# Performance work log

Hardware: AMD Instinct MI355X
Metric: run time of the kernel (lower is better)

The kernel has to match this reference:

```python
import jax, jax.numpy as jnp
import numpy as np

N_NODES = 50000
N_EDGES = 800000
IN = 128
HID = 128
OUT = 128
EDGE_F = 2
EPS = 1e-30


def _linear_params(key, fan_in, fan_out, bias=True):
    k1, k2 = jax.random.split(key)
    bound = 1.0 / np.sqrt(fan_in)
    W = jax.random.uniform(k1, (fan_in, fan_out), jnp.float32, -bound, bound)
    if bias:
        b = jax.random.uniform(k2, (fan_out,), jnp.float32, -bound, bound)
        return W, b
    return (W,)


def setup_inputs() -> dict:
    key = jax.random.key(0)
    ks = jax.random.split(key, 12)
    node_feat = jax.random.normal(ks[0], (N_NODES, IN), jnp.float32)
    coord_feat = jax.random.normal(ks[1], (N_NODES, 3), jnp.float32)
    edge_feat = jax.random.normal(ks[2], (N_EDGES, EDGE_F), jnp.float32)
    src = jax.random.randint(ks[3], (N_EDGES,), 0, N_NODES, jnp.int32)
    dst = jax.random.randint(ks[4], (N_EDGES,), 0, N_NODES, jnp.int32)
    # edge_mlp: Linear(2*IN+EDGE_F+1 -> HID), SiLU, Linear(HID -> HID), SiLU
    eW1, eb1 = _linear_params(ks[5], 2 * IN + EDGE_F + 1, HID)
    eW2, eb2 = _linear_params(ks[6], HID, HID)
    # node_mlp: Linear(IN+HID -> HID), SiLU, Linear(HID -> OUT)
    nW1, nb1 = _linear_params(ks[7], IN + HID, HID)
    nW2, nb2 = _linear_params(ks[8], HID, OUT)
    # coord_mlp: Linear(HID -> HID), SiLU, Linear(HID -> 1, bias=False)
    cW1, cb1 = _linear_params(ks[9], HID, HID)
    (cW2,) = _linear_params(ks[10], HID, 1, bias=False)
    return {
        "node_feat": node_feat, "coord_feat": coord_feat, "edge_feat": edge_feat,
        "src": src, "dst": dst,
        "eW1": eW1, "eb1": eb1, "eW2": eW2, "eb2": eb2,
        "nW1": nW1, "nb1": nb1, "nW2": nW2, "nb2": nb2,
        "cW1": cW1, "cb1": cb1, "cW2": cW2,
    }


def reference(node_feat, coord_feat, edge_feat, src, dst,
              eW1, eb1, eW2, eb2, nW1, nb1, nW2, nb2, cW1, cb1, cW2):
    silu = jax.nn.silu
    n = node_feat.shape[0]
    # per-edge gathers (src -> dst message flow, as in DGL)
    h_src = node_feat[src]                      # [E, IN]
    h_dst = node_feat[dst]                      # [E, IN]
    x_diff = coord_feat[src] - coord_feat[dst]  # [E, 3]
    radial = jnp.sum(x_diff * x_diff, axis=1, keepdims=True)  # [E, 1]
    x_diff = x_diff / (jnp.sqrt(radial) + EPS)
    # edge MLP
    f = jnp.concatenate([h_src, h_dst, radial, edge_feat], axis=-1)  # [E, 2*IN+1+EF]
    msg_h = silu(silu(f @ eW1 + eb1) @ eW2 + eb2)                    # [E, HID]
    msg_x = (silu(msg_h @ cW1 + cb1) @ cW2) * x_diff                 # [E, 3]
    # scatter to destination nodes: sum for h, mean for x
    h_neigh = jax.ops.segment_sum(msg_h, dst, num_segments=n)        # [N, HID]
    x_sum = jax.ops.segment_sum(msg_x, dst, num_segments=n)          # [N, 3]
    deg = jax.ops.segment_sum(jnp.ones((msg_x.shape[0],), msg_x.dtype), dst, num_segments=n)
    x_neigh = x_sum / jnp.maximum(deg, 1.0)[:, None]
    # node update
    h = silu(jnp.concatenate([node_feat, h_neigh], axis=-1) @ nW1 + nb1) @ nW2 + nb2
    x = coord_feat + x_neigh
    return h, x
```

## Files before the change

kernel.cpp:

```cpp
#include <hip/hip_runtime.h>
#include <hip/hip_bf16.h>

#define N_NODES 50000
#define E_TOTAL 800000
#define IN      128
#define HID     128
#define EPB     64
#define XOFF    ((size_t)N_NODES * HID)
#define FP      296
#define H1OFF   160
#define HP      136
#define CP      264

typedef __attribute__((ext_vector_type(8))) short short8v;
typedef __attribute__((ext_vector_type(4))) float f32x4;

__device__ __forceinline__ float silu_f(float x) { return x / (1.0f + __expf(-x)); }

__device__ __forceinline__ uint pkbf(float lo, float hi) {
    float2 f; f.x = lo; f.y = hi;
    __hip_bfloat162 h = __float22bfloat162_rn(f);
    union { __hip_bfloat162 h; uint u; } c; c.h = h;
    return c.u;
}

__device__ __forceinline__ ushort f2bf(float x) {
    uint u = __float_as_uint(x);
    u += 0x7fff + ((u >> 16) & 1);
    return (ushort)(u >> 16);
}

__global__ __launch_bounds__(256) void prep_kernel(
    const float* __restrict__ eW1, const float* __restrict__ eW2,
    const float* __restrict__ cW1, const float* __restrict__ nW1,
    const float* __restrict__ nW2, const float* __restrict__ node_feat,
    ushort* __restrict__ pk1, ushort* __restrict__ pk2, ushort* __restrict__ pk3,
    ushort* __restrict__ pkn1, ushort* __restrict__ pkn2,
    ushort* __restrict__ nfb, int do_nfb)
{
    int id = blockIdx.x * 256 + threadIdx.x;
    if (id < 14848) {
        const float* W; ushort* dp; int K, idx;
        if (id < 4608)       { idx = id;         W = eW1; dp = pk1;  K = 259; }
        else if (id < 6656)  { idx = id - 4608;  W = eW2; dp = pk2;  K = 128; }
        else if (id < 8704)  { idx = id - 6656;  W = cW1; dp = pk3;  K = 128; }
        else if (id < 12800) { idx = id - 8704;  W = nW1; dp = pkn1; K = 256; }
        else                 { idx = id - 12800; W = nW2; dp = pkn2; K = 128; }
        int kt = idx >> 9, n = (idx >> 6) & 7, ll = idx & 63;
        int col = (n << 4) + (ll & 15);
        short8v o;
#pragma unroll
        for (int j = 0; j < 8; ++j) {
            int k = (kt << 5) + ((ll >> 4) << 3) + j;
            o[j] = (k < K) ? (short)f2bf(W[(size_t)k * 128 + col]) : (short)0;
        }
        *reinterpret_cast<short8v*>(dp + (size_t)idx * 8) = o;
    } else if (do_nfb) {
        int idx = id - 14848;
        if (idx < N_NODES * 16) {
            const float4* s = reinterpret_cast<const float4*>(node_feat + (size_t)idx * 8);
            float4 a = s[0], b = s[1];
            uint4 u;
            u.x = pkbf(a.x, a.y); u.y = pkbf(a.z, a.w);
            u.z = pkbf(b.x, b.y); u.w = pkbf(b.z, b.w);
            *reinterpret_cast<uint4*>(nfb + (size_t)idx * 8) = u;
        }
    }
}

template<bool NFB>
__global__ __launch_bounds__(512, 8) void edge_kernel(
    const float* __restrict__ node_feat, const ushort* __restrict__ nfb,
    const float* __restrict__ coord, const float* __restrict__ edge_feat,
    const int* __restrict__ src, const int* __restrict__ dst,
    const ushort* __restrict__ pk1, const ushort* __restrict__ pk2,
    const ushort* __restrict__ pk3,
    const float* __restrict__ eb1, const float* __restrict__ eb2,
    const float* __restrict__ cb1, const float* __restrict__ cW2,
    float* __restrict__ hacc, float* __restrict__ xacc, float* __restrict__ deg)
{
    __shared__ __attribute__((aligned(16))) ushort fbuf[EPB][FP];
    __shared__ int   sbuf[EPB], dbuf[EPB];
    __shared__ float xdbuf[EPB][4];
    __shared__ float pbuf[4][EPB];

    const int t   = threadIdx.x;
    const int l   = t & 63;
    const int w   = t >> 6;
    const int ch  = w & 3;
    const int eh  = w >> 2;
    const int r16 = l & 15;
    const int g   = l >> 4;
    const int e_base = blockIdx.x * EPB;

    if (t < EPB) { sbuf[t] = src[e_base + t]; dbuf[t] = dst[e_base + t]; }
    __syncthreads();

    {
        const int e = t >> 3;
        const int c = (t & 7) << 5;
        if (NFB) {
            const ushort* sp = (c < 128) ? nfb + (size_t)sbuf[e] * 128 + c
                                         : nfb + (size_t)dbuf[e] * 128 + (c - 128);
            const short8v* spv = reinterpret_cast<const short8v*>(sp);
#pragma unroll
            for (int i = 0; i < 4; ++i)
                *reinterpret_cast<short8v*>(&fbuf[e][c + (i << 3)]) = spv[i];
        } else {
            const float* sp = (c < 128) ? node_feat + (size_t)sbuf[e] * 128 + c
                                        : node_feat + (size_t)dbuf[e] * 128 + (c - 128);
            const float4* spv = reinterpret_cast<const float4*>(sp);
#pragma unroll
            for (int i = 0; i < 4; ++i) {
                float4 a = spv[2 * i], b = spv[2 * i + 1];
                uint4 u;
                u.x = pkbf(a.x, a.y); u.y = pkbf(a.z, a.w);
                u.z = pkbf(b.x, b.y); u.w = pkbf(b.z, b.w);
                *reinterpret_cast<uint4*>(&fbuf[e][c + (i << 3)]) = u;
            }
        }
    }
    if (t < EPB) {
        const int e = t, s = sbuf[e], d = dbuf[e];
        float dx = coord[(size_t)s*3+0] - coord[(size_t)d*3+0];
        float dy = coord[(size_t)s*3+1] - coord[(size_t)d*3+1];
        float dz = coord[(size_t)s*3+2] - coord[(size_t)d*3+2];
        float radial = dx*dx + dy*dy + dz*dz;
        float inv = 1.0f / (sqrtf(radial) + 1e-30f);
        fbuf[e][256] = f2bf(radial);
        fbuf[e][257] = f2bf(edge_feat[(size_t)(e_base + e)*2 + 0]);
        fbuf[e][258] = f2bf(edge_feat[(size_t)(e_base + e)*2 + 1]);
#pragma unroll
        for (int k = 259; k < 288; ++k) fbuf[e][k] = 0;
        xdbuf[e][0] = dx * inv; xdbuf[e][1] = dy * inv; xdbuf[e][2] = dz * inv;
    }
    __syncthreads();

    const f32x4 zero = {0.f, 0.f, 0.f, 0.f};
    const short8v* pkv1 = reinterpret_cast<const short8v*>(pk1);
    const short8v* pkv2 = reinterpret_cast<const short8v*>(pk2);
    const short8v* pkv3 = reinterpret_cast<const short8v*>(pk3);

    f32x4 acc[2][2];
    acc[0][0] = zero; acc[0][1] = zero; acc[1][0] = zero; acc[1][1] = zero;
    for (int kt = 0; kt < 9; ++kt) {
        short8v b0 = *reinterpret_cast<const short8v*>(&fbuf[(eh << 5) + r16][(kt << 5) + (g << 3)]);
        short8v b1 = *reinterpret_cast<const short8v*>(&fbuf[(eh << 5) + 16 + r16][(kt << 5) + (g << 3)]);
#pragma unroll
        for (int nt = 0; nt < 2; ++nt) {
            short8v a = pkv1[(((kt << 3) + (ch << 1) + nt) << 6) + l];
            acc[0][nt] = __builtin_amdgcn_mfma_f32_16x16x32_bf16(a, b0, acc[0][nt], 0, 0, 0);
            acc[1][nt] = __builtin_amdgcn_mfma_f32_16x16x32_bf16(a, b1, acc[1][nt], 0, 0, 0);
        }
    }
    __syncthreads();
#pragma unroll
    for (int nt = 0; nt < 2; ++nt) {
        int cb = (ch << 5) + (nt << 4) + (g << 2);
        float4 bias = *reinterpret_cast<const float4*>(&eb1[cb]);
#pragma unroll
        for (int et = 0; et < 2; ++et) {
            int e = (eh << 5) + (et << 4) + r16;
            f32x4 v = acc[et][nt];
            uint2 p;
            p.x = pkbf(silu_f(v[0] + bias.x), silu_f(v[1] + bias.y));
            p.y = pkbf(silu_f(v[2] + bias.z), silu_f(v[3] + bias.w));
            *reinterpret_cast<uint2*>(&fbuf[e][H1OFF + cb]) = p;
        }
    }
    __syncthreads();

    acc[0][0] = zero; acc[0][1] = zero; acc[1][0] = zero; acc[1][1] = zero;
    for (int kt = 0; kt < 4; ++kt) {
        short8v b0 = *reinterpret_cast<const short8v*>(&fbuf[(eh << 5) + r16][H1OFF + (kt << 5) + (g << 3)]);
        short8v b1 = *reinterpret_cast<const short8v*>(&fbuf[(eh << 5) + 16 + r16][H1OFF + (kt << 5) + (g << 3)]);
#pragma unroll
        for (int nt = 0; nt < 2; ++nt) {
            short8v a = pkv2[(((kt << 3) + (ch << 1) + nt) << 6) + l];
            acc[0][nt] = __builtin_amdgcn_mfma_f32_16x16x32_bf16(a, b0, acc[0][nt], 0, 0, 0);
            acc[1][nt] = __builtin_amdgcn_mfma_f32_16x16x32_bf16(a, b1, acc[1][nt], 0, 0, 0);
        }
    }
#pragma unroll
    for (int nt = 0; nt < 2; ++nt) {
        int cb = (ch << 5) + (nt << 4) + (g << 2);
        float4 bias = *reinterpret_cast<const float4*>(&eb2[cb]);
#pragma unroll
        for (int et = 0; et < 2; ++et) {
            int e = (eh << 5) + (et << 4) + r16;
            f32x4 v = acc[et][nt];
            uint2 p;
            p.x = pkbf(silu_f(v[0] + bias.x), silu_f(v[1] + bias.y));
            p.y = pkbf(silu_f(v[2] + bias.z), silu_f(v[3] + bias.w));
            *reinterpret_cast<uint2*>(&fbuf[e][cb]) = p;
        }
    }
    __syncthreads();

    {
        const int se = t >> 4;
        const int sc = t & 15;
#pragma unroll
        for (int p = 0; p < 2; ++p) {
            int e = se + (p << 5);
            int gd = dbuf[e];
            float* dp = hacc + (size_t)gd * HID + sc;
#pragma unroll
            for (int i = 0; i < 8; ++i) {
                ushort us = fbuf[e][sc + (i << 4)];
                atomicAdd(dp + (i << 4), __uint_as_float((uint)us << 16));
            }
        }
    }

    acc[0][0] = zero; acc[0][1] = zero; acc[1][0] = zero; acc[1][1] = zero;
    for (int kt = 0; kt < 4; ++kt) {
        short8v b0 = *reinterpret_cast<const short8v*>(&fbuf[(eh << 5) + r16][(kt << 5) + (g << 3)]);
        short8v b1 = *reinterpret_cast<const short8v*>(&fbuf[(eh << 5) + 16 + r16][(kt << 5) + (g << 3)]);
#pragma unroll
        for (int nt = 0; nt < 2; ++nt) {
            short8v a = pkv3[(((kt << 3) + (ch << 1) + nt) << 6) + l];
            acc[0][nt] = __builtin_amdgcn_mfma_f32_16x16x32_bf16(a, b0, acc[0][nt], 0, 0, 0);
            acc[1][nt] = __builtin_amdgcn_mfma_f32_16x16x32_bf16(a, b1, acc[1][nt], 0, 0, 0);
        }
    }
    float part[2] = {0.f, 0.f};
#pragma unroll
    for (int nt = 0; nt < 2; ++nt) {
        int cb = (ch << 5) + (nt << 4) + (g << 2);
        float4 bias = *reinterpret_cast<const float4*>(&cb1[cb]);
        float4 cw   = *reinterpret_cast<const float4*>(&cW2[cb]);
#pragma unroll
        for (int et = 0; et < 2; ++et) {
            f32x4 v = acc[et][nt];
            part[et] += silu_f(v[0] + bias.x) * cw.x + silu_f(v[1] + bias.y) * cw.y
                      + silu_f(v[2] + bias.z) * cw.z + silu_f(v[3] + bias.w) * cw.w;
        }
    }
#pragma unroll
    for (int et = 0; et < 2; ++et) {
        part[et] += __shfl_xor(part[et], 16);
        part[et] += __shfl_xor(part[et], 32);
    }
    if (l < 16) {
        pbuf[ch][(eh << 5) + r16]      = part[0];
        pbuf[ch][(eh << 5) + 16 + r16] = part[1];
    }
    __syncthreads();

    if (t < EPB) {
        float s = pbuf[0][t] + pbuf[1][t] + pbuf[2][t] + pbuf[3][t];
        int gd = dbuf[t];
        atomicAdd(&xacc[(size_t)gd*3 + 0], s * xdbuf[t][0]);
        atomicAdd(&xacc[(size_t)gd*3 + 1], s * xdbuf[t][1]);
        atomicAdd(&xacc[(size_t)gd*3 + 2], s * xdbuf[t][2]);
        atomicAdd(&deg[gd], 1.0f);
    }
}

template<bool NFB>
__global__ __launch_bounds__(256) void node_kernel(
    const float* __restrict__ node_feat, const ushort* __restrict__ nfb,
    const float* __restrict__ coord,
    const ushort* __restrict__ pkn1, const ushort* __restrict__ pkn2,
    const float* __restrict__ nb1, const float* __restrict__ nb2,
    float* __restrict__ dout, const float* __restrict__ deg)
{
    __shared__ __attribute__((aligned(16))) ushort catb[32][CP];
    __shared__ __attribute__((aligned(16))) ushort h1b[32][HP];

    const int t   = threadIdx.x;
    const int l   = t & 63;
    const int w   = t >> 6;
    const int ch  = w & 1;
    const int eh  = w >> 1;
    const int r16 = l & 15;
    const int g   = l >> 4;
    const int nb  = blockIdx.x * 32;

    {
        int nd = t >> 3;
        int c  = (t & 7) << 5;
        int gn = nb + nd; if (gn >= N_NODES) gn = N_NODES - 1;
        if (c < 128) {
            if (NFB) {
                const short8v* spv = reinterpret_cast<const short8v*>(nfb + (size_t)gn * 128 + c);
#pragma unroll
                for (int i = 0; i < 4; ++i)
                    *reinterpret_cast<short8v*>(&catb[nd][c + (i << 3)]) = spv[i];
            } else {
                const float4* spv = reinterpret_cast<const float4*>(node_feat + (size_t)gn * 128 + c);
#pragma unroll
                for (int i = 0; i < 4; ++i) {
                    float4 a = spv[2 * i], b = spv[2 * i + 1];
                    uint4 u;
                    u.x = pkbf(a.x, a.y); u.y = pkbf(a.z, a.w);
                    u.z = pkbf(b.x, b.y); u.w = pkbf(b.z, b.w);
                    *reinterpret_cast<uint4*>(&catb[nd][c + (i << 3)]) = u;
                }
            }
        } else {
            const float4* spv = reinterpret_cast<const float4*>(dout + (size_t)gn * HID + (c - 128));
#pragma unroll
            for (int i = 0; i < 4; ++i) {
                float4 a = spv[2 * i], b = spv[2 * i + 1];
                uint4 u;
                u.x = pkbf(a.x, a.y); u.y = pkbf(a.z, a.w);
                u.z = pkbf(b.x, b.y); u.w = pkbf(b.z, b.w);
                *reinterpret_cast<uint4*>(&catb[nd][c + (i << 3)]) = u;
            }
        }
    }
    __syncthreads();

    const f32x4 zero = {0.f, 0.f, 0.f, 0.f};
    const short8v* pv1 = reinterpret_cast<const short8v*>(pkn1);
    const short8v* pv2 = reinterpret_cast<const short8v*>(pkn2);

    f32x4 acc[4];
#pragma unroll
    for (int nt = 0; nt < 4; ++nt) acc[nt] = zero;
    for (int kt = 0; kt < 8; ++kt) {
        short8v b = *reinterpret_cast<const short8v*>(&catb[(eh << 4) + r16][(kt << 5) + (g << 3)]);
#pragma unroll
        for (int nt = 0; nt < 4; ++nt) {
            short8v a = pv1[(((kt << 3) + (ch << 2) + nt) << 6) + l];
            acc[nt] = __builtin_amdgcn_mfma_f32_16x16x32_bf16(a, b, acc[nt], 0, 0, 0);
        }
    }
#pragma unroll
    for (int nt = 0; nt < 4; ++nt) {
        int cb = (ch << 6) + (nt << 4) + (g << 2);
        float4 bias = *reinterpret_cast<const float4*>(&nb1[cb]);
        int nd = (eh << 4) + r16;
        f32x4 v = acc[nt];
        uint2 p;
        p.x = pkbf(silu_f(v[0] + bias.x), silu_f(v[1] + bias.y));
        p.y = pkbf(silu_f(v[2] + bias.z), silu_f(v[3] + bias.w));
        *reinterpret_cast<uint2*>(&h1b[nd][cb]) = p;
    }
    __syncthreads();

#pragma unroll
    for (int nt = 0; nt < 4; ++nt) acc[nt] = zero;
    for (int kt = 0; kt < 4; ++kt) {
        short8v b = *reinterpret_cast<const short8v*>(&h1b[(eh << 4) + r16][(kt << 5) + (g << 3)]);
#pragma unroll
        for (int nt = 0; nt < 4; ++nt) {
            short8v a = pv2[(((kt << 3) + (ch << 2) + nt) << 6) + l];
            acc[nt] = __builtin_amdgcn_mfma_f32_16x16x32_bf16(a, b, acc[nt], 0, 0, 0);
        }
    }
    {
        int gw = nb + (eh << 4) + r16;
        if (gw < N_NODES) {
#pragma unroll
            for (int nt = 0; nt < 4; ++nt) {
                int cb = (ch << 6) + (nt << 4) + (g << 2);
                float4 bias = *reinterpret_cast<const float4*>(&nb2[cb]);
                f32x4 v = acc[nt];
                float4 o;
                o.x = v[0] + bias.x; o.y = v[1] + bias.y;
                o.z = v[2] + bias.z; o.w = v[3] + bias.w;
                *reinterpret_cast<float4*>(&dout[(size_t)gw * HID + cb]) = o;
            }
        }
    }

    if (t < 96) {
        int nd = t / 3, d = t - 3 * nd;
        int gn = nb + nd;
        if (gn < N_NODES) {
            size_t xi = XOFF + (size_t)gn * 3 + d;
            float dg = deg[gn];
            dg = dg > 1.0f ? dg : 1.0f;
            dout[xi] = coord[(size_t)gn * 3 + d] + dout[xi] / dg;
        }
    }
}

extern "C" void kernel_launch(void* const* d_in, const int* in_sizes, int n_in,
                              void* d_out, int out_size, void* d_ws, size_t ws_size,
                              hipStream_t stream) {
    const float* node_feat = (const float*)d_in[0];
    const float* coord     = (const float*)d_in[1];
    const float* edge_feat = (const float*)d_in[2];
    const int*   src       = (const int*)d_in[3];
    const int*   dst       = (const int*)d_in[4];
    const float* eW1 = (const float*)d_in[5];
    const float* eb1 = (const float*)d_in[6];
    const float* eW2 = (const float*)d_in[7];
    const float* eb2 = (const float*)d_in[8];
    const float* nW1 = (const float*)d_in[9];
    const float* nb1 = (const float*)d_in[10];
    const float* nW2 = (const float*)d_in[11];
    const float* nb2 = (const float*)d_in[12];
    const float* cW1 = (const float*)d_in[13];
    const float* cb1 = (const float*)d_in[14];
    const float* cW2 = (const float*)d_in[15];

    float* out = (float*)d_out;
    float* deg = (float*)d_ws;
    char* base = (char*)d_ws;
    ushort* pk1  = (ushort*)(base + 200000);
    ushort* pk2  = (ushort*)(base + 273728);
    ushort* pk3  = (ushort*)(base + 306496);
    ushort* pkn1 = (ushort*)(base + 339264);
    ushort* pkn2 = (ushort*)(base + 404800);
    ushort* nfb  = (ushort*)(base + 437568);
    const size_t need_nfb = 437568 + (size_t)N_NODES * 128 * 2;
    const bool use_nfb = ws_size >= need_nfb;

    hipMemsetAsync(d_out, 0, (size_t)out_size * sizeof(float), stream);
    hipMemsetAsync(d_ws, 0, 200000, stream);

    int prep_grid = use_nfb ? (14848 + N_NODES * 16 + 255) / 256 : 58;
    prep_kernel<<<prep_grid, 256, 0, stream>>>(
        eW1, eW2, cW1, nW1, nW2, node_feat,
        pk1, pk2, pk3, pkn1, pkn2, nfb, use_nfb ? 1 : 0);

    if (use_nfb) {
        edge_kernel<true><<<E_TOTAL / EPB, 512, 0, stream>>>(
            node_feat, nfb, coord, edge_feat, src, dst,
            pk1, pk2, pk3, eb1, eb2, cb1, cW2, out, out + XOFF, deg);
        node_kernel<true><<<(N_NODES + 31) / 32, 256, 0, stream>>>(
            node_feat, nfb, coord, pkn1, pkn2, nb1, nb2, out, deg);
    } else {
        edge_kernel<false><<<E_TOTAL / EPB, 512, 0, stream>>>(
            node_feat, nfb, coord, edge_feat, src, dst,
            pk1, pk2, pk3, eb1, eb2, cb1, cW2, out, out + XOFF, deg);
        node_kernel<false><<<(N_NODES + 31) / 32, 256, 0, stream>>>(
            node_feat, nfb, coord, pkn1, pkn2, nb1, nb2, out, deg);
    }
}
```

Before: 551.8 us.

## Sort edges by destination via counting sort and segment-reduce scatter atomics

Adds histogram, single-block scan and scatter kernels that build a CSR pointer array and a permutation of edges grouped by destination. The edge kernel walks edges in that order and, in the h scatter, sums runs of identical destinations in registers before each atomic, so fewer global float atomics are issued. The degree now comes from the CSR pointers instead of per-edge atomics. The cost is three extra launches, a serial one-block scan over all nodes, and node and edge gathers that become less coalesced through the permutation.

```diff
diff --git a/kernel.cpp b/kernel.cpp
--- a/kernel.cpp
+++ b/kernel.cpp
@@ -68,16 +68,72 @@
     }
 }
 
+__global__ __launch_bounds__(256) void hist_kernel(
+    const int* __restrict__ dst, int* __restrict__ cnt)
+{
+    int e = blockIdx.x * 256 + threadIdx.x;
+    if (e < E_TOTAL) atomicAdd(&cnt[dst[e]], 1);
+}
+
+__global__ __launch_bounds__(1024) void scan_kernel(
+    int* __restrict__ ptr, int* __restrict__ ptr2)
+{
+    __shared__ int wsum[16];
+    __shared__ int carry_s;
+    const int t = threadIdx.x, lane = t & 63, wv = t >> 6;
+    if (t == 0) carry_s = 0;
+    __syncthreads();
+    for (int base = 0; base < N_NODES; base += 1024) {
+        int v = (base + t < N_NODES) ? ptr[base + t] : 0;
+        int x = v;
+#pragma unroll
+        for (int off = 1; off < 64; off <<= 1) {
+            int y = __shfl_up(x, off);
+            if (lane >= off) x += y;
+        }
+        if (lane == 63) wsum[wv] = x;
+        __syncthreads();
+        if (wv == 0) {
+            int s = (lane < 16) ? wsum[lane] : 0;
+#pragma unroll
+            for (int off = 1; off < 16; off <<= 1) {
+                int y = __shfl_up(s, off);
+                if (lane >= off) s += y;
+            }
+            if (lane < 16) wsum[lane] = s;
+        }
+        __syncthreads();
+        int wbase = (wv == 0) ? 0 : wsum[wv - 1];
+        int excl = carry_s + wbase + x - v;
+        if (base + t < N_NODES) { ptr[base + t] = excl; ptr2[base + t] = excl; }
+        __syncthreads();
+        if (t == 1023) carry_s += wsum[15];
+        __syncthreads();
+    }
+    if (t == 0) { ptr[N_NODES] = E_TOTAL; ptr2[N_NODES] = E_TOTAL; }
+}
+
+__global__ __launch_bounds__(256) void scatter_kernel(
+    const int* __restrict__ dst, int* __restrict__ ptr2, int* __restrict__ perm)
+{
+    int e = blockIdx.x * 256 + threadIdx.x;
+    if (e < E_TOTAL) {
+        int p = atomicAdd(&ptr2[dst[e]], 1);
+        perm[p] = e;
+    }
+}
+
 template<bool NFB>
 __global__ __launch_bounds__(512, 8) void edge_kernel(
     const float* __restrict__ node_feat, const ushort* __restrict__ nfb,
     const float* __restrict__ coord, const float* __restrict__ edge_feat,
     const int* __restrict__ src, const int* __restrict__ dst,
+    const int* __restrict__ perm, int use_perm,
     const ushort* __restrict__ pk1, const ushort* __restrict__ pk2,
     const ushort* __restrict__ pk3,
     const float* __restrict__ eb1, const float* __restrict__ eb2,
     const float* __restrict__ cb1, const float* __restrict__ cW2,
-    float* __restrict__ hacc, float* __restrict__ xacc, float* __restrict__ deg)
+    float* __restrict__ hacc, float* __restrict__ xacc)
 {
     __shared__ __attribute__((aligned(16))) ushort fbuf[EPB][FP];
     __shared__ int   sbuf[EPB], dbuf[EPB];
@@ -93,7 +149,12 @@
     const int g   = l >> 4;
     const int e_base = blockIdx.x * EPB;
 
-    if (t < EPB) { sbuf[t] = src[e_base + t]; dbuf[t] = dst[e_base + t]; }
+    int ee = 0;
+    if (t < EPB) {
+        ee = use_perm ? perm[e_base + t] : (e_base + t);
+        sbuf[t] = src[ee];
+        dbuf[t] = dst[ee];
+    }
     __syncthreads();
 
     {
@@ -128,8 +189,8 @@
         float radial = dx*dx + dy*dy + dz*dz;
         float inv = 1.0f / (sqrtf(radial) + 1e-30f);
         fbuf[e][256] = f2bf(radial);
-        fbuf[e][257] = f2bf(edge_feat[(size_t)(e_base + e)*2 + 0]);
-        fbuf[e][258] = f2bf(edge_feat[(size_t)(e_base + e)*2 + 1]);
+        fbuf[e][257] = f2bf(edge_feat[(size_t)ee*2 + 0]);
+        fbuf[e][258] = f2bf(edge_feat[(size_t)ee*2 + 1]);
 #pragma unroll
         for (int k = 259; k < 288; ++k) fbuf[e][k] = 0;
         xdbuf[e][0] = dx * inv; xdbuf[e][1] = dy * inv; xdbuf[e][2] = dz * inv;
@@ -198,17 +259,18 @@
     __syncthreads();
 
     {
-        const int se = t >> 4;
-        const int sc = t & 15;
-#pragma unroll
-        for (int p = 0; p < 2; ++p) {
-            int e = se + (p << 5);
-            int gd = dbuf[e];
-            float* dp = hacc + (size_t)gd * HID + sc;
-#pragma unroll
-            for (int i = 0; i < 8; ++i) {
-                ushort us = fbuf[e][sc + (i << 4)];
-                atomicAdd(dp + (i << 4), __uint_as_float((uint)us << 16));
+        const int c = t & 127;
+        const int q = t >> 7;
+        float sum = 0.f;
+        int cur = dbuf[q << 4];
+#pragma unroll
+        for (int i = 0; i < 16; ++i) {
+            int e = (q << 4) + i;
+            sum += __uint_as_float((uint)fbuf[e][c] << 16);
+            int nxt = (i < 15) ? dbuf[e + 1] : -1;
+            if (nxt != cur) {
+                atomicAdd(&hacc[(size_t)cur * HID + c], sum);
+                sum = 0.f; cur = nxt;
             }
         }
     }
@@ -254,7 +316,6 @@
         atomicAdd(&xacc[(size_t)gd*3 + 0], s * xdbuf[t][0]);
         atomicAdd(&xacc[(size_t)gd*3 + 1], s * xdbuf[t][1]);
         atomicAdd(&xacc[(size_t)gd*3 + 2], s * xdbuf[t][2]);
-        atomicAdd(&deg[gd], 1.0f);
     }
 }
 
@@ -264,7 +325,7 @@
     const float* __restrict__ coord,
     const ushort* __restrict__ pkn1, const ushort* __restrict__ pkn2,
     const float* __restrict__ nb1, const float* __restrict__ nb2,
-    float* __restrict__ dout, const float* __restrict__ deg)
+    float* __restrict__ dout, const int* __restrict__ ptr)
 {
     __shared__ __attribute__((aligned(16))) ushort catb[32][CP];
     __shared__ __attribute__((aligned(16))) ushort h1b[32][HP];
@@ -372,7 +433,7 @@
         int gn = nb + nd;
         if (gn < N_NODES) {
             size_t xi = XOFF + (size_t)gn * 3 + d;
-            float dg = deg[gn];
+            float dg = (float)(ptr[gn + 1] - ptr[gn]);
             dg = dg > 1.0f ? dg : 1.0f;
             dout[xi] = coord[(size_t)gn * 3 + d] + dout[xi] / dg;
         }
@@ -400,36 +461,43 @@
     const float* cW2 = (const float*)d_in[15];
 
     float* out = (float*)d_out;
-    float* deg = (float*)d_ws;
     char* base = (char*)d_ws;
-    ushort* pk1  = (ushort*)(base + 200000);
-    ushort* pk2  = (ushort*)(base + 273728);
-    ushort* pk3  = (ushort*)(base + 306496);
-    ushort* pkn1 = (ushort*)(base + 339264);
-    ushort* pkn2 = (ushort*)(base + 404800);
-    ushort* nfb  = (ushort*)(base + 437568);
-    const size_t need_nfb = 437568 + (size_t)N_NODES * 128 * 2;
-    const bool use_nfb = ws_size >= need_nfb;
+    int*    ptrb = (int*)base;
+    int*    ptr2 = (int*)(base + 200064);
+    ushort* pk1  = (ushort*)(base + 400128);
+    ushort* pk2  = (ushort*)(base + 473856);
+    ushort* pk3  = (ushort*)(base + 506624);
+    ushort* pkn1 = (ushort*)(base + 539392);
+    ushort* pkn2 = (ushort*)(base + 604928);
+    int*    perm = (int*)(base + 637696);
+    ushort* nfb  = (ushort*)(base + 3837696);
+    const bool use_perm = ws_size >= 3837696;
+    const bool use_nfb  = ws_size >= 16637696;
 
     hipMemsetAsync(d_out, 0, (size_t)out_size * sizeof(float), stream);
-    hipMemsetAsync(d_ws, 0, 200000, stream);
+    hipMemsetAsync(d_ws, 0, 200064, stream);
 
     int prep_grid = use_nfb ? (14848 + N_NODES * 16 + 255) / 256 : 58;
     prep_kernel<<<prep_grid, 256, 0, stream>>>(
         eW1, eW2, cW1, nW1, nW2, node_feat,
         pk1, pk2, pk3, pkn1, pkn2, nfb, use_nfb ? 1 : 0);
 
+    hist_kernel<<<(E_TOTAL + 255) / 256, 256, 0, stream>>>(dst, ptrb);
+    scan_kernel<<<1, 1024, 0, stream>>>(ptrb, ptr2);
+    if (use_perm)
+        scatter_kernel<<<(E_TOTAL + 255) / 256, 256, 0, stream>>>(dst, ptr2, perm);
+
     if (use_nfb) {
         edge_kernel<true><<<E_TOTAL / EPB, 512, 0, stream>>>(
-            node_feat, nfb, coord, edge_feat, src, dst,
-            pk1, pk2, pk3, eb1, eb2, cb1, cW2, out, out + XOFF, deg);
+            node_feat, nfb, coord, edge_feat, src, dst, perm, use_perm ? 1 : 0,
+            pk1, pk2, pk3, eb1, eb2, cb1, cW2, out, out + XOFF);
         node_kernel<true><<<(N_NODES + 31) / 32, 256, 0, stream>>>(
-            node_feat, nfb, coord, pkn1, pkn2, nb1, nb2, out, deg);
+            node_feat, nfb, coord, pkn1, pkn2, nb1, nb2, out, ptrb);
     } else {
         edge_kernel<false><<<E_TOTAL / EPB, 512, 0, stream>>>(
-            node_feat, nfb, coord, edge_feat, src, dst,
-            pk1, pk2, pk3, eb1, eb2, cb1, cW2, out, out + XOFF, deg);
+            node_feat, nfb, coord, edge_feat, src, dst, perm, use_perm ? 1 : 0,
+            pk1, pk2, pk3, eb1, eb2, cb1, cW2, out, out + XOFF);
         node_kernel<false><<<(N_NODES + 31) / 32, 256, 0, stream>>>(
-            node_feat, nfb, coord, pkn1, pkn2, nb1, nb2, out, deg);
-    }
-}
+            node_feat, nfb, coord, pkn1, pkn2, nb1, nb2, out, ptrb);
+    }
+}
```

Measured after the change: 553.7 us. About the same (+0.3%).
